# Kernel tuning notes

Measured on AMD Instinct MI355X. Metric: run time of the kernel, lower is better.

The kernel has to match this reference:

```python
import jax, jax.numpy as jnp
import numpy as np

B, S = 64, 1024
D_INPUT, D_POLAR, N_LAYERS, KAN, N_CLASSES = 256, 256, 8, 32, 1000
PI = float(np.pi)
EPS = 1e-8


def _gelu(v):
    return jax.nn.gelu(v, approximate=False)  # torch nn.GELU default = exact erf


def setup_inputs() -> dict:
    key = jax.random.key(0)
    ks = jax.random.split(key, 16)

    def rn(k, shape, fan_in):
        return jax.random.normal(k, shape, jnp.float32) / np.sqrt(fan_in)

    return {
        "x": jax.random.normal(ks[0], (B, S, D_INPUT), jnp.float32),
        "embed_w": rn(ks[1], (D_INPUT, 2 * D_POLAR), D_INPUT),
        "embed_b": jnp.zeros((2 * D_POLAR,), jnp.float32),
        "mag_w1": rn(ks[2], (N_LAYERS, 1, KAN), 1),
        "mag_b1": jnp.zeros((N_LAYERS, KAN), jnp.float32),
        "mag_w2": rn(ks[3], (N_LAYERS, KAN, 1), KAN),
        "mag_b2": jnp.zeros((N_LAYERS, 1), jnp.float32),
        "ph_w1": rn(ks[4], (N_LAYERS, 2, KAN), 2),
        "ph_b1": jnp.zeros((N_LAYERS, KAN), jnp.float32),
        "ph_w2": rn(ks[5], (N_LAYERS, KAN, 2), KAN),
        "ph_b2": jnp.zeros((N_LAYERS, 2), jnp.float32),
        "cls_w1": rn(ks[6], (D_POLAR, KAN), D_POLAR),
        "cls_b1": jnp.zeros((KAN,), jnp.float32),
        "cls_w2": rn(ks[7], (KAN, N_CLASSES), KAN),
        "cls_b2": jnp.zeros((N_CLASSES,), jnp.float32),
    }


def _forward(x, embed_w, embed_b, mag_w1, mag_b1, mag_w2, mag_b2,
             ph_w1, ph_b1, ph_w2, ph_b2, cls_w1, cls_b1, cls_w2, cls_b2):
    h = x @ embed_w + embed_b                      # [B,S,2D]
    r = jnp.abs(h[..., :D_POLAR]) + 0.1            # [B,S,D]
    theta = h[..., D_POLAR:] * PI                  # [B,S,D]
    for i in range(N_LAYERS):
        xc = r * jnp.cos(theta)
        yc = r * jnp.sin(theta)
        xm = xc.mean(axis=1, keepdims=True)        # [B,1,D]
        ym = yc.mean(axis=1, keepdims=True)
        r_agg = jnp.sqrt(xm * xm + ym * ym + EPS)
        th_agg = jnp.arctan2(ym, xm)
        # magnitude MLP (1 -> 32 -> 1) in log space, per channel
        log_r = jnp.log(r_agg + EPS)[..., None]    # [B,1,D,1]
        lr = _gelu(log_r @ mag_w1[i] + mag_b1[i]) @ mag_w2[i] + mag_b2[i]
        r_trans = jnp.exp(lr[..., 0])              # [B,1,D]
        # phase MLP (2 -> 32 -> 2) on (sin, cos)
        pin = jnp.stack([jnp.sin(th_agg), jnp.cos(th_agg)], axis=-1)  # [B,1,D,2]
        pout = _gelu(pin @ ph_w1[i] + ph_b1[i]) @ ph_w2[i] + ph_b2[i]
        norm = jnp.sqrt(pout[..., 0] ** 2 + pout[..., 1] ** 2 + EPS)
        th_trans = jnp.arctan2(pout[..., 0] / norm, pout[..., 1] / norm)
        x_out = xc + r_trans * jnp.cos(th_trans)
        y_out = yc + r_trans * jnp.sin(th_trans)
        r = jnp.sqrt(x_out * x_out + y_out * y_out + EPS)
        theta = jnp.arctan2(y_out, x_out)
    pooled = r.mean(axis=1)                        # [B,D]
    return _gelu(pooled @ cls_w1 + cls_b1) @ cls_w2 + cls_b2  # [B,n_classes]


def reference(x, embed_w, embed_b, mag_w1, mag_b1, mag_w2, mag_b2,
              ph_w1, ph_b1, ph_w2, ph_b2, cls_w1, cls_b1, cls_w2, cls_b2):
    return _forward(x, embed_w, embed_b, mag_w1, mag_b1, mag_w2, mag_b2,
                    ph_w1, ph_b1, ph_w2, ph_b2, cls_w1, cls_b1, cls_w2, cls_b2)
```

## Files before the change

### kernel.cpp

```cpp
#include <hip/hip_runtime.h>
#include <hip/hip_bf16.h>
#include <hip/hip_fp16.h>

#define EPS 1e-8f
#define PI_F 3.14159265358979323846f

typedef _Float16 half8 __attribute__((ext_vector_type(8)));
typedef _Float16 half4 __attribute__((ext_vector_type(4)));
typedef float f32x4 __attribute__((ext_vector_type(4)));
typedef float f32x2 __attribute__((ext_vector_type(2)));

__device__ __forceinline__ float gelu_exact(float v) {
    return 0.5f * v * (1.0f + erff(v * 0.70710678118654752f));
}

__global__ void convertW(const float* __restrict__ W,
                         _Float16* __restrict__ Wth, _Float16* __restrict__ Wtl,
                         float* __restrict__ zero_base) {
    int idx = blockIdx.x * 256 + threadIdx.x;
    if (idx < 49152) zero_base[idx] = 0.f;
    int col = idx & 511, k = idx >> 9;
    int d   = col & 255;
    int g   = d >> 6;
    int dl  = d & 63;
    int h12 = col >> 8;
    int r   = (dl >> 5) * 64 + ((dl & 1) + 2 * h12) * 16 + ((dl & 31) >> 1);
    int kt  = k >> 5, ko = k & 31;
    float f = W[k * 512 + col];
    _Float16 h = (_Float16)f;
    int o = ((g * 8 + kt) * 128 + r) * 32 + ko;
    Wth[o] = h;
    Wtl[o] = (_Float16)(f - (float)h);
}

__global__ __launch_bounds__(256) void gemm_embed(
    const float* __restrict__ x,
    const _Float16* __restrict__ Wth, const _Float16* __restrict__ Wtl,
    const float* __restrict__ bias,
    unsigned short* __restrict__ XY8,
    float* __restrict__ XMsum, float* __restrict__ YMsum)
{
    const int tid  = threadIdx.x;
    const int wave = tid >> 6;
    const int lane = tid & 63;
    const int wm   = wave >> 1;
    const int wn   = wave & 1;
    const int id   = blockIdx.x;
    const int xcd  = id & 7;
    const int s    = id >> 3;
    const int g    = s & 3;
    const int mt   = (s >> 2) * 8 + xcd;
    const int m0   = mt * 128;
    const int q    = lane >> 4, ln = lane & 15;

    f32x4 acc[4][4];
#pragma unroll
    for (int mi = 0; mi < 4; ++mi)
#pragma unroll
        for (int nt = 0; nt < 4; ++nt)
            acc[mi][nt] = (f32x4){0.f, 0.f, 0.f, 0.f};

    const float* xbase[4];
#pragma unroll
    for (int mi = 0; mi < 4; ++mi)
        xbase[mi] = x + (size_t)(m0 + wm * 64 + mi * 16 + ln) * 256 + q * 8;

    const _Float16* wb = Wth + (size_t)g * 32768 + (wn * 64 + ln) * 32 + q * 8;
    const _Float16* wl = Wtl + (size_t)g * 32768 + (wn * 64 + ln) * 32 + q * 8;

#pragma unroll 1
    for (int kt = 0; kt < 8; ++kt) {
        half8 bh[4], bl[4];
#pragma unroll
        for (int nt = 0; nt < 4; ++nt) {
            bh[nt] = *(const half8*)(wb + kt * 4096 + nt * 512);
            bl[nt] = *(const half8*)(wl + kt * 4096 + nt * 512);
        }
#pragma unroll
        for (int mi = 0; mi < 4; ++mi) {
            const float* src = xbase[mi] + kt * 32;
            const float4 f0 = *(const float4*)(src);
            const float4 f1 = *(const float4*)(src + 4);
            half8 hh, ll;
            hh[0] = (_Float16)f0.x; ll[0] = (_Float16)(f0.x - (float)hh[0]);
            hh[1] = (_Float16)f0.y; ll[1] = (_Float16)(f0.y - (float)hh[1]);
            hh[2] = (_Float16)f0.z; ll[2] = (_Float16)(f0.z - (float)hh[2]);
            hh[3] = (_Float16)f0.w; ll[3] = (_Float16)(f0.w - (float)hh[3]);
            hh[4] = (_Float16)f1.x; ll[4] = (_Float16)(f1.x - (float)hh[4]);
            hh[5] = (_Float16)f1.y; ll[5] = (_Float16)(f1.y - (float)hh[5]);
            hh[6] = (_Float16)f1.z; ll[6] = (_Float16)(f1.z - (float)hh[6]);
            hh[7] = (_Float16)f1.w; ll[7] = (_Float16)(f1.w - (float)hh[7]);
#pragma unroll
            for (int nt = 0; nt < 4; ++nt)
                acc[mi][nt] = __builtin_amdgcn_mfma_f32_16x16x32_f16(hh, bh[nt], acc[mi][nt], 0, 0, 0);
#pragma unroll
            for (int nt = 0; nt < 4; ++nt)
                acc[mi][nt] = __builtin_amdgcn_mfma_f32_16x16x32_f16(hh, bl[nt], acc[mi][nt], 0, 0, 0);
#pragma unroll
            for (int nt = 0; nt < 4; ++nt)
                acc[mi][nt] = __builtin_amdgcn_mfma_f32_16x16x32_f16(ll, bh[nt], acc[mi][nt], 0, 0, 0);
        }
    }

    const int d0 = g * 64 + wn * 32 + 2 * ln;
    const int b  = m0 >> 10;
    const float b1_0 = bias[d0],       b1_1 = bias[d0 + 1];
    const float b2_0 = bias[256 + d0], b2_1 = bias[256 + d0 + 1];
    float sx0 = 0.f, sy0 = 0.f, sx1 = 0.f, sy1 = 0.f;
#pragma unroll
    for (int mi = 0; mi < 4; ++mi) {
#pragma unroll
        for (int i = 0; i < 4; ++i) {
            const int row = m0 + wm * 64 + mi * 16 + q * 4 + i;
            const float h1a = acc[mi][0][i] + b1_0;
            const float h2a = acc[mi][2][i] + b2_0;
            const float rra = fabsf(h1a) + 0.1f;
            float sva, cva;
            __sincosf(PI_F * h2a, &sva, &cva);
            const float xca = rra * cva, yca = rra * sva;
            const float h1b = acc[mi][1][i] + b1_1;
            const float h2b = acc[mi][3][i] + b2_1;
            const float rrb = fabsf(h1b) + 0.1f;
            float svb, cvb;
            __sincosf(PI_F * h2b, &svb, &cvb);
            const float xcb = rrb * cvb, ycb = rrb * svb;
            int pk = __builtin_amdgcn_cvt_pk_fp8_f32(xca, yca, 0, false);
            pk = __builtin_amdgcn_cvt_pk_fp8_f32(xcb, ycb, pk, true);
            *(unsigned int*)(XY8 + (size_t)row * 256 + d0) = (unsigned int)pk;
            sx0 += xca; sy0 += yca;
            sx1 += xcb; sy1 += ycb;
        }
    }
    sx0 += __shfl_down(sx0, 32); sx0 += __shfl_down(sx0, 16);
    sy0 += __shfl_down(sy0, 32); sy0 += __shfl_down(sy0, 16);
    sx1 += __shfl_down(sx1, 32); sx1 += __shfl_down(sx1, 16);
    sy1 += __shfl_down(sy1, 32); sy1 += __shfl_down(sy1, 16);
    if (lane < 16) {
        atomicAdd(&XMsum[b * 256 + d0], sx0);
        atomicAdd(&YMsum[b * 256 + d0], sy0);
        atomicAdd(&XMsum[b * 256 + d0 + 1], sx1);
        atomicAdd(&YMsum[b * 256 + d0 + 1], sy1);
    }
}

__global__ __launch_bounds__(256) void layers_kernel(
    const float* __restrict__ XMsum, const float* __restrict__ YMsum,
    const float* __restrict__ mw1, const float* __restrict__ mb1,
    const float* __restrict__ mw2, const float* __restrict__ mb2,
    const float* __restrict__ pw1, const float* __restrict__ pb1,
    const float* __restrict__ pw2, const float* __restrict__ pb2,
    float* __restrict__ DX, float* __restrict__ DY)
{
    __shared__ float s_mw1[256], s_mb1[256], s_mw2[256], s_mb2[8];
    __shared__ float s_pw1[512], s_pb1[256], s_pw2[512], s_pb2[16];
    const int tid = threadIdx.x;
    s_mw1[tid] = mw1[tid]; s_mb1[tid] = mb1[tid];
    s_mw2[tid] = mw2[tid]; s_pb1[tid] = pb1[tid];
    s_pw1[tid] = pw1[tid]; s_pw1[256 + tid] = pw1[256 + tid];
    s_pw2[tid] = pw2[tid]; s_pw2[256 + tid] = pw2[256 + tid];
    if (tid < 8)  s_mb2[tid] = mb2[tid];
    if (tid < 16) s_pb2[tid] = pb2[tid];
    __syncthreads();

    const int gid = blockIdx.x * 256 + tid;
    const int idx = gid >> 3;
    const int sub = gid & 7;
    float xm = XMsum[idx] * (1.0f / 1024.0f);
    float ym = YMsum[idx] * (1.0f / 1024.0f);
    float dxa = 0.f, dya = 0.f;
#pragma unroll 1
    for (int i = 0; i < 8; ++i) {
        float r2    = xm * xm + ym * ym;
        float r_agg = sqrtf(r2 + EPS);
        float hyp   = sqrtf(r2);
        float inv   = hyp > 0.f ? 1.0f / hyp : 0.f;
        float st    = ym * inv;
        float ct    = hyp > 0.f ? xm * inv : 1.0f;
        float log_r = logf(r_agg + EPS);
        float lr = 0.f, p0 = 0.f, p1 = 0.f;
#pragma unroll
        for (int k4 = 0; k4 < 4; ++k4) {
            int k = sub * 4 + k4;
            float hm = gelu_exact(log_r * s_mw1[i * 32 + k] + s_mb1[i * 32 + k]);
            lr += hm * s_mw2[i * 32 + k];
            float hp = gelu_exact(st * s_pw1[i * 64 + k] + ct * s_pw1[i * 64 + 32 + k] + s_pb1[i * 32 + k]);
            p0 += hp * s_pw2[i * 64 + 2 * k + 0];
            p1 += hp * s_pw2[i * 64 + 2 * k + 1];
        }
        lr += __shfl_xor(lr, 1); lr += __shfl_xor(lr, 2); lr += __shfl_xor(lr, 4);
        p0 += __shfl_xor(p0, 1); p0 += __shfl_xor(p0, 2); p0 += __shfl_xor(p0, 4);
        p1 += __shfl_xor(p1, 1); p1 += __shfl_xor(p1, 2); p1 += __shfl_xor(p1, 4);
        lr += s_mb2[i];
        p0 += s_pb2[i * 2 + 0];
        p1 += s_pb2[i * 2 + 1];
        float r_trans = expf(lr);
        float hp2  = sqrtf(p0 * p0 + p1 * p1);
        float invp = hp2 > 0.f ? 1.0f / hp2 : 0.f;
        float ctt  = hp2 > 0.f ? p1 * invp : 1.0f;
        float stt  = p0 * invp;
        float dx = r_trans * ctt;
        float dy = r_trans * stt;
        dxa += dx; dya += dy; xm += dx; ym += dy;
    }
    if (sub == 0) { DX[idx] = dxa; DY[idx] = dya; }
}

__global__ __launch_bounds__(256) void pool_kernel(
    const unsigned short* __restrict__ XY8,
    const float* __restrict__ DX, const float* __restrict__ DY,
    float* __restrict__ pooled)
{
    __shared__ float red[256][9];
    const int b = blockIdx.x, sc = blockIdx.y, tid = threadIdx.x;
    const int dg = tid & 31;
    const int sh = tid >> 5;
    const int d0 = dg * 8;
    float dxv[8], dyv[8], s[8];
#pragma unroll
    for (int j = 0; j < 8; ++j) {
        dxv[j] = DX[b * 256 + d0 + j];
        dyv[j] = DY[b * 256 + d0 + j];
        s[j] = 0.f;
    }
    const int r0 = sc * 128 + sh * 16;
    const size_t base = ((size_t)b * 1024 + r0) * 256 + d0;
#pragma unroll 4
    for (int i = 0; i < 16; ++i) {
        const int4 v = *(const int4*)(XY8 + base + (size_t)i * 256);
        const int wv[4] = {v.x, v.y, v.z, v.w};
#pragma unroll
        for (int w = 0; w < 4; ++w) {
            f32x2 pa = __builtin_amdgcn_cvt_pk_f32_fp8(wv[w], false);
            f32x2 pb = __builtin_amdgcn_cvt_pk_f32_fp8(wv[w], true);
            float xa = pa[0] + dxv[2 * w],     ya = pa[1] + dyv[2 * w];
            float xb = pb[0] + dxv[2 * w + 1], yb = pb[1] + dyv[2 * w + 1];
            s[2 * w]     += sqrtf(xa * xa + ya * ya + EPS);
            s[2 * w + 1] += sqrtf(xb * xb + yb * yb + EPS);
        }
    }
#pragma unroll
    for (int j = 0; j < 8; ++j) red[tid][j] = s[j];
    __syncthreads();
    if (tid < 32) {
#pragma unroll
        for (int j = 0; j < 8; ++j) {
            float t = 0.f;
#pragma unroll
            for (int c = 0; c < 8; ++c) t += red[c * 32 + tid][j];
            atomicAdd(&pooled[b * 256 + tid * 8 + j], t);
        }
    }
}

__global__ __launch_bounds__(256) void cls_kernel(
    const float* __restrict__ pooled,
    const float* __restrict__ w1, const float* __restrict__ b1,
    const float* __restrict__ w2, const float* __restrict__ b2,
    float* __restrict__ out)
{
    __shared__ float pl[256];
    __shared__ float part[8][32];
    __shared__ float hd[32];
    const int b = blockIdx.x, yc = blockIdx.y, tid = threadIdx.x;
    pl[tid] = pooled[b * 256 + tid] * (1.0f / 1024.0f);
    __syncthreads();
    const int hu = tid & 31, kc = tid >> 5;
    float a = 0.f;
    for (int k = kc * 32; k < kc * 32 + 32; ++k) a += pl[k] * w1[k * 32 + hu];
    part[kc][hu] = a;
    __syncthreads();
    if (tid < 32) {
        float s = b1[tid];
#pragma unroll
        for (int c = 0; c < 8; ++c) s += part[c][tid];
        hd[tid] = gelu_exact(s);
    }
    __syncthreads();
    const int n0 = yc * 250;
    const int nend = (n0 + 250 < 1000) ? n0 + 250 : 1000;
    for (int n = n0 + tid; n < nend; n += 256) {
        float s = b2[n];
#pragma unroll
        for (int k = 0; k < 32; ++k) s += hd[k] * w2[k * 1000 + n];
        out[b * 1000 + n] = s;
    }
}

extern "C" void kernel_launch(void* const* d_in, const int* in_sizes, int n_in,
                              void* d_out, int out_size, void* d_ws, size_t ws_size,
                              hipStream_t stream)
{
    const float* x       = (const float*)d_in[0];
    const float* embed_w = (const float*)d_in[1];
    const float* embed_b = (const float*)d_in[2];
    const float* mag_w1  = (const float*)d_in[3];
    const float* mag_b1  = (const float*)d_in[4];
    const float* mag_w2  = (const float*)d_in[5];
    const float* mag_b2  = (const float*)d_in[6];
    const float* ph_w1   = (const float*)d_in[7];
    const float* ph_b1   = (const float*)d_in[8];
    const float* ph_w2   = (const float*)d_in[9];
    const float* ph_b2   = (const float*)d_in[10];
    const float* cls_w1  = (const float*)d_in[11];
    const float* cls_b1  = (const float*)d_in[12];
    const float* cls_w2  = (const float*)d_in[13];
    const float* cls_b2  = (const float*)d_in[14];
    float* out = (float*)d_out;

    char* ws = (char*)d_ws;
    unsigned short* XY8 = (unsigned short*)(ws + 0);
    _Float16* Wth = (_Float16*)(ws + 33554432);
    _Float16* Wtl = (_Float16*)(ws + 33816576);
    float* XMsum  = (float*)(ws + 34078720);
    float* YMsum  = (float*)(ws + 34144256);
    float* pooled = (float*)(ws + 34209792);
    float* DX     = (float*)(ws + 34275328);
    float* DY     = (float*)(ws + 34340864);

    convertW<<<512, 256, 0, stream>>>(embed_w, Wth, Wtl, XMsum);
    gemm_embed<<<2048, 256, 0, stream>>>(x, Wth, Wtl, embed_b, XY8, XMsum, YMsum);
    layers_kernel<<<512, 256, 0, stream>>>(XMsum, YMsum, mag_w1, mag_b1, mag_w2, mag_b2,
                                           ph_w1, ph_b1, ph_w2, ph_b2, DX, DY);
    pool_kernel<<<dim3(64, 8), 256, 0, stream>>>(XY8, DX, DY, pooled);
    cls_kernel<<<dim3(64, 4), 256, 0, stream>>>(pooled, cls_w1, cls_b1, cls_w2, cls_b2, out);
}
```

Measured before the change: 239.5 us.

## Stage embed GEMM input tiles through double-buffered swizzled LDS with async loads

The embedding GEMM previously had each wave read its fp32 x rows straight from global memory, so the two column-waves sharing a row block fetched the same data twice. Now the whole 128x32 fp32 tile is copied once per block into LDS with global_load_lds, using an XOR swizzle to avoid bank conflicts. Two LDS buffers let the next k-step's copy run while the current one is being converted and fed to MFMA. The launch bounds also now request 4 blocks per CU. The cost is 32 KB of LDS per block and a barrier each k-step, both of which may limit occupancy.

```diff
diff --git a/kernel.cpp b/kernel.cpp
--- a/kernel.cpp
+++ b/kernel.cpp
@@ -12,6 +12,12 @@
 
 __device__ __forceinline__ float gelu_exact(float v) {
     return 0.5f * v * (1.0f + erff(v * 0.70710678118654752f));
+}
+
+__device__ __forceinline__ void load_lds16(const float* g, float* l) {
+    __builtin_amdgcn_global_load_lds(
+        (const __attribute__((address_space(1))) void*)g,
+        (__attribute__((address_space(3))) void*)l, 16, 0, 0);
 }
 
 __global__ void convertW(const float* __restrict__ W,
@@ -33,13 +39,14 @@
     Wtl[o] = (_Float16)(f - (float)h);
 }
 
-__global__ __launch_bounds__(256) void gemm_embed(
+__global__ __launch_bounds__(256, 4) void gemm_embed(
     const float* __restrict__ x,
     const _Float16* __restrict__ Wth, const _Float16* __restrict__ Wtl,
     const float* __restrict__ bias,
     unsigned short* __restrict__ XY8,
     float* __restrict__ XMsum, float* __restrict__ YMsum)
 {
+    __shared__ __attribute__((aligned(16))) float A32[2][4096];
     const int tid  = threadIdx.x;
     const int wave = tid >> 6;
     const int lane = tid & 63;
@@ -60,27 +67,44 @@
         for (int nt = 0; nt < 4; ++nt)
             acc[mi][nt] = (f32x4){0.f, 0.f, 0.f, 0.f};
 
-    const float* xbase[4];
-#pragma unroll
-    for (int mi = 0; mi < 4; ++mi)
-        xbase[mi] = x + (size_t)(m0 + wm * 64 + mi * 16 + ln) * 256 + q * 8;
+    const float* srcp[4];
+#pragma unroll
+    for (int n = 0; n < 4; ++n) {
+        const int G  = wave * 256 + n * 64 + lane;
+        const int r  = G >> 3;
+        const int gp = G & 7;
+        srcp[n] = x + (size_t)(m0 + r) * 256 + ((gp ^ (r & 7)) * 4);
+    }
+
+#define STAGE(KT, C)                                                          \
+    {                                                                         \
+        float* lb_ = &A32[C][wave * 1024];                                    \
+        _Pragma("unroll")                                                     \
+        for (int n = 0; n < 4; ++n)                                           \
+            load_lds16(srcp[n] + (KT) * 32, lb_ + n * 256);                   \
+    }
 
     const _Float16* wb = Wth + (size_t)g * 32768 + (wn * 64 + ln) * 32 + q * 8;
     const _Float16* wl = Wtl + (size_t)g * 32768 + (wn * 64 + ln) * 32 + q * 8;
 
+    STAGE(0, 0);
+
 #pragma unroll 1
     for (int kt = 0; kt < 8; ++kt) {
+        const int c = kt & 1;
         half8 bh[4], bl[4];
 #pragma unroll
         for (int nt = 0; nt < 4; ++nt) {
             bh[nt] = *(const half8*)(wb + kt * 4096 + nt * 512);
             bl[nt] = *(const half8*)(wl + kt * 4096 + nt * 512);
         }
+        __syncthreads();
+        if (kt < 7) STAGE(kt + 1, c ^ 1);
 #pragma unroll
         for (int mi = 0; mi < 4; ++mi) {
-            const float* src = xbase[mi] + kt * 32;
-            const float4 f0 = *(const float4*)(src);
-            const float4 f1 = *(const float4*)(src + 4);
+            const int r = wm * 64 + mi * 16 + ln;
+            const float4 f0 = *(const float4*)&A32[c][r * 32 + ((2 * q)     ^ (r & 7)) * 4];
+            const float4 f1 = *(const float4*)&A32[c][r * 32 + ((2 * q + 1) ^ (r & 7)) * 4];
             half8 hh, ll;
             hh[0] = (_Float16)f0.x; ll[0] = (_Float16)(f0.x - (float)hh[0]);
             hh[1] = (_Float16)f0.y; ll[1] = (_Float16)(f0.y - (float)hh[1]);
@@ -101,6 +125,7 @@
                 acc[mi][nt] = __builtin_amdgcn_mfma_f32_16x16x32_f16(ll, bh[nt], acc[mi][nt], 0, 0, 0);
         }
     }
+#undef STAGE
 
     const int d0 = g * 64 + wn * 32 + 2 * ln;
     const int b  = m0 >> 10;
```

New measurement: 210.7 us. 12.0% less time.

## Fuse all stages into one cooperative persistent kernel and stage A tiles through LDS

Applied to the files above, without the earlier changes.

Replaces the five separate launches with a single cooperative kernel of 1024 blocks that runs weight conversion, GEMM, layers, pooling and the classifier, separated by grid-wide syncs, with the old multi-launch path kept as a fallback if the cooperative launch fails. The GEMM now has each block cooperatively load and split the x tile into fp16 hi/lo parts in swizzled shared memory, then read MFMA fragments from there instead of every wave converting its own rows. The aim is to cut launch gaps and redundant global loads and conversions. In exchange it adds grid-sync overhead, leaves most blocks idle in the later phases, and caps occupancy with launch bounds of 4 blocks per CU.

```diff
diff --git a/kernel.cpp b/kernel.cpp
--- a/kernel.cpp
+++ b/kernel.cpp
@@ -1,12 +1,14 @@
 #include <hip/hip_runtime.h>
+#include <hip/hip_cooperative_groups.h>
 #include <hip/hip_bf16.h>
 #include <hip/hip_fp16.h>
 
 #define EPS 1e-8f
 #define PI_F 3.14159265358979323846f
 
+namespace cg = cooperative_groups;
+
 typedef _Float16 half8 __attribute__((ext_vector_type(8)));
-typedef _Float16 half4 __attribute__((ext_vector_type(4)));
 typedef float f32x4 __attribute__((ext_vector_type(4)));
 typedef float f32x2 __attribute__((ext_vector_type(2)));
 
@@ -14,10 +16,12 @@
     return 0.5f * v * (1.0f + erff(v * 0.70710678118654752f));
 }
 
-__global__ void convertW(const float* __restrict__ W,
-                         _Float16* __restrict__ Wth, _Float16* __restrict__ Wtl,
-                         float* __restrict__ zero_base) {
-    int idx = blockIdx.x * 256 + threadIdx.x;
+
+__device__ __forceinline__ void convert_body(
+    int idx, const float* __restrict__ W,
+    _Float16* __restrict__ Wth, _Float16* __restrict__ Wtl,
+    float* __restrict__ zero_base)
+{
     if (idx < 49152) zero_base[idx] = 0.f;
     int col = idx & 511, k = idx >> 9;
     int d   = col & 255;
@@ -33,19 +37,18 @@
     Wtl[o] = (_Float16)(f - (float)h);
 }
 
-__global__ __launch_bounds__(256) void gemm_embed(
+__device__ __forceinline__ void gemm_unit(
+    int id, int tid, _Float16* Ah, _Float16* Al,
     const float* __restrict__ x,
     const _Float16* __restrict__ Wth, const _Float16* __restrict__ Wtl,
     const float* __restrict__ bias,
     unsigned short* __restrict__ XY8,
     float* __restrict__ XMsum, float* __restrict__ YMsum)
 {
-    const int tid  = threadIdx.x;
     const int wave = tid >> 6;
     const int lane = tid & 63;
     const int wm   = wave >> 1;
     const int wn   = wave & 1;
-    const int id   = blockIdx.x;
     const int xcd  = id & 7;
     const int s    = id >> 3;
     const int g    = s & 3;
@@ -60,11 +63,6 @@
         for (int nt = 0; nt < 4; ++nt)
             acc[mi][nt] = (f32x4){0.f, 0.f, 0.f, 0.f};
 
-    const float* xbase[4];
-#pragma unroll
-    for (int mi = 0; mi < 4; ++mi)
-        xbase[mi] = x + (size_t)(m0 + wm * 64 + mi * 16 + ln) * 256 + q * 8;
-
     const _Float16* wb = Wth + (size_t)g * 32768 + (wn * 64 + ln) * 32 + q * 8;
     const _Float16* wl = Wtl + (size_t)g * 32768 + (wn * 64 + ln) * 32 + q * 8;
 
@@ -76,9 +74,12 @@
             bh[nt] = *(const half8*)(wb + kt * 4096 + nt * 512);
             bl[nt] = *(const half8*)(wl + kt * 4096 + nt * 512);
         }
-#pragma unroll
-        for (int mi = 0; mi < 4; ++mi) {
-            const float* src = xbase[mi] + kt * 32;
+        __syncthreads();
+#pragma unroll
+        for (int L = 0; L < 2; ++L) {
+            int idx2 = L * 256 + tid;
+            int r = idx2 >> 2, cq = idx2 & 3;
+            const float* src = x + (size_t)(m0 + r) * 256 + kt * 32 + cq * 8;
             const float4 f0 = *(const float4*)(src);
             const float4 f1 = *(const float4*)(src + 4);
             half8 hh, ll;
@@ -90,15 +91,35 @@
             hh[5] = (_Float16)f1.y; ll[5] = (_Float16)(f1.y - (float)hh[5]);
             hh[6] = (_Float16)f1.z; ll[6] = (_Float16)(f1.z - (float)hh[6]);
             hh[7] = (_Float16)f1.w; ll[7] = (_Float16)(f1.w - (float)hh[7]);
+            int pos = cq ^ ((r >> 1) & 3);
+            *(half8*)&Ah[r * 32 + pos * 8] = hh;
+            *(half8*)&Al[r * 32 + pos * 8] = ll;
+        }
+        __syncthreads();
+
+        half8 am[4];
+#pragma unroll
+        for (int mi = 0; mi < 4; ++mi) {
+            int row = wm * 64 + mi * 16 + ln;
+            am[mi] = *(const half8*)&Ah[row * 32 + (q ^ ((row >> 1) & 3)) * 8];
+        }
+#pragma unroll
+        for (int mi = 0; mi < 4; ++mi)
 #pragma unroll
             for (int nt = 0; nt < 4; ++nt)
-                acc[mi][nt] = __builtin_amdgcn_mfma_f32_16x16x32_f16(hh, bh[nt], acc[mi][nt], 0, 0, 0);
+                acc[mi][nt] = __builtin_amdgcn_mfma_f32_16x16x32_f16(am[mi], bh[nt], acc[mi][nt], 0, 0, 0);
+#pragma unroll
+        for (int mi = 0; mi < 4; ++mi)
 #pragma unroll
             for (int nt = 0; nt < 4; ++nt)
-                acc[mi][nt] = __builtin_amdgcn_mfma_f32_16x16x32_f16(hh, bl[nt], acc[mi][nt], 0, 0, 0);
+                acc[mi][nt] = __builtin_amdgcn_mfma_f32_16x16x32_f16(am[mi], bl[nt], acc[mi][nt], 0, 0, 0);
+#pragma unroll
+        for (int mi = 0; mi < 4; ++mi) {
+            int row = wm * 64 + mi * 16 + ln;
+            half8 alv = *(const half8*)&Al[row * 32 + (q ^ ((row >> 1) & 3)) * 8];
 #pragma unroll
             for (int nt = 0; nt < 4; ++nt)
-                acc[mi][nt] = __builtin_amdgcn_mfma_f32_16x16x32_f16(ll, bh[nt], acc[mi][nt], 0, 0, 0);
+                acc[mi][nt] = __builtin_amdgcn_mfma_f32_16x16x32_f16(alv, bh[nt], acc[mi][nt], 0, 0, 0);
         }
     }
 
@@ -143,7 +164,8 @@
     }
 }
 
-__global__ __launch_bounds__(256) void layers_kernel(
+__device__ __forceinline__ void layers_body(
+    int bid, int tid, float* sm,
     const float* __restrict__ XMsum, const float* __restrict__ YMsum,
     const float* __restrict__ mw1, const float* __restrict__ mb1,
     const float* __restrict__ mw2, const float* __restrict__ mb2,
@@ -151,18 +173,15 @@
     const float* __restrict__ pw2, const float* __restrict__ pb2,
     float* __restrict__ DX, float* __restrict__ DY)
 {
-    __shared__ float s_mw1[256], s_mb1[256], s_mw2[256], s_mb2[8];
-    __shared__ float s_pw1[512], s_pb1[256], s_pw2[512], s_pb2[16];
-    const int tid = threadIdx.x;
-    s_mw1[tid] = mw1[tid]; s_mb1[tid] = mb1[tid];
-    s_mw2[tid] = mw2[tid]; s_pb1[tid] = pb1[tid];
-    s_pw1[tid] = pw1[tid]; s_pw1[256 + tid] = pw1[256 + tid];
-    s_pw2[tid] = pw2[tid]; s_pw2[256 + tid] = pw2[256 + tid];
-    if (tid < 8)  s_mb2[tid] = mb2[tid];
-    if (tid < 16) s_pb2[tid] = pb2[tid];
+    sm[tid] = mw1[tid]; sm[256 + tid] = mb1[tid];
+    sm[512 + tid] = mw2[tid]; sm[768 + tid] = pb1[tid];
+    sm[1024 + tid] = pw1[tid]; sm[1280 + tid] = pw1[256 + tid];
+    sm[1536 + tid] = pw2[tid]; sm[1792 + tid] = pw2[256 + tid];
+    if (tid < 8)  sm[2048 + tid] = mb2[tid];
+    if (tid < 16) sm[2056 + tid] = pb2[tid];
     __syncthreads();
 
-    const int gid = blockIdx.x * 256 + tid;
+    const int gid = bid * 256 + tid;
     const int idx = gid >> 3;
     const int sub = gid & 7;
     float xm = XMsum[idx] * (1.0f / 1024.0f);
@@ -181,18 +200,18 @@
 #pragma unroll
         for (int k4 = 0; k4 < 4; ++k4) {
             int k = sub * 4 + k4;
-            float hm = gelu_exact(log_r * s_mw1[i * 32 + k] + s_mb1[i * 32 + k]);
-            lr += hm * s_mw2[i * 32 + k];
-            float hp = gelu_exact(st * s_pw1[i * 64 + k] + ct * s_pw1[i * 64 + 32 + k] + s_pb1[i * 32 + k]);
-            p0 += hp * s_pw2[i * 64 + 2 * k + 0];
-            p1 += hp * s_pw2[i * 64 + 2 * k + 1];
+            float hm = gelu_exact(log_r * sm[i * 32 + k] + sm[256 + i * 32 + k]);
+            lr += hm * sm[512 + i * 32 + k];
+            float hp = gelu_exact(st * sm[1024 + i * 64 + k] + ct * sm[1024 + i * 64 + 32 + k] + sm[768 + i * 32 + k]);
+            p0 += hp * sm[1536 + i * 64 + 2 * k + 0];
+            p1 += hp * sm[1536 + i * 64 + 2 * k + 1];
         }
         lr += __shfl_xor(lr, 1); lr += __shfl_xor(lr, 2); lr += __shfl_xor(lr, 4);
         p0 += __shfl_xor(p0, 1); p0 += __shfl_xor(p0, 2); p0 += __shfl_xor(p0, 4);
         p1 += __shfl_xor(p1, 1); p1 += __shfl_xor(p1, 2); p1 += __shfl_xor(p1, 4);
-        lr += s_mb2[i];
-        p0 += s_pb2[i * 2 + 0];
-        p1 += s_pb2[i * 2 + 1];
+        lr += sm[2048 + i];
+        p0 += sm[2056 + i * 2 + 0];
+        p1 += sm[2056 + i * 2 + 1];
         float r_trans = expf(lr);
         float hp2  = sqrtf(p0 * p0 + p1 * p1);
         float invp = hp2 > 0.f ? 1.0f / hp2 : 0.f;
@@ -205,13 +224,12 @@
     if (sub == 0) { DX[idx] = dxa; DY[idx] = dya; }
 }
 
-__global__ __launch_bounds__(256) void pool_kernel(
+__device__ __forceinline__ void pool_body(
+    int b, int sc, int tid, float (*red)[9],
     const unsigned short* __restrict__ XY8,
     const float* __restrict__ DX, const float* __restrict__ DY,
     float* __restrict__ pooled)
 {
-    __shared__ float red[256][9];
-    const int b = blockIdx.x, sc = blockIdx.y, tid = threadIdx.x;
     const int dg = tid & 31;
     const int sh = tid >> 5;
     const int d0 = dg * 8;
@@ -252,28 +270,25 @@
     }
 }
 
-__global__ __launch_bounds__(256) void cls_kernel(
+__device__ __forceinline__ void cls_body(
+    int b, int yc, int tid, float* smf,
     const float* __restrict__ pooled,
     const float* __restrict__ w1, const float* __restrict__ b1,
     const float* __restrict__ w2, const float* __restrict__ b2,
     float* __restrict__ out)
 {
-    __shared__ float pl[256];
-    __shared__ float part[8][32];
-    __shared__ float hd[32];
-    const int b = blockIdx.x, yc = blockIdx.y, tid = threadIdx.x;
-    pl[tid] = pooled[b * 256 + tid] * (1.0f / 1024.0f);
+    smf[tid] = pooled[b * 256 + tid] * (1.0f / 1024.0f);
     __syncthreads();
     const int hu = tid & 31, kc = tid >> 5;
     float a = 0.f;
-    for (int k = kc * 32; k < kc * 32 + 32; ++k) a += pl[k] * w1[k * 32 + hu];
-    part[kc][hu] = a;
+    for (int k = kc * 32; k < kc * 32 + 32; ++k) a += smf[k] * w1[k * 32 + hu];
+    smf[256 + kc * 32 + hu] = a;
     __syncthreads();
     if (tid < 32) {
         float s = b1[tid];
 #pragma unroll
-        for (int c = 0; c < 8; ++c) s += part[c][tid];
-        hd[tid] = gelu_exact(s);
+        for (int c = 0; c < 8; ++c) s += smf[256 + c * 32 + tid];
+        smf[512 + tid] = gelu_exact(s);
     }
     __syncthreads();
     const int n0 = yc * 250;
@@ -281,9 +296,105 @@
     for (int n = n0 + tid; n < nend; n += 256) {
         float s = b2[n];
 #pragma unroll
-        for (int k = 0; k < 32; ++k) s += hd[k] * w2[k * 1000 + n];
+        for (int k = 0; k < 32; ++k) s += smf[512 + k] * w2[k * 1000 + n];
         out[b * 1000 + n] = s;
     }
+}
+
+__global__ __launch_bounds__(256, 4) void fused_all(
+    const float* __restrict__ x, const float* __restrict__ embed_w,
+    const float* __restrict__ embed_b,
+    const float* __restrict__ mw1, const float* __restrict__ mb1,
+    const float* __restrict__ mw2, const float* __restrict__ mb2,
+    const float* __restrict__ pw1, const float* __restrict__ pb1,
+    const float* __restrict__ pw2, const float* __restrict__ pb2,
+    const float* __restrict__ cw1, const float* __restrict__ cb1,
+    const float* __restrict__ cw2, const float* __restrict__ cb2,
+    float* __restrict__ out,
+    unsigned short* __restrict__ XY8,
+    _Float16* __restrict__ Wth, _Float16* __restrict__ Wtl,
+    float* __restrict__ XMsum, float* __restrict__ YMsum,
+    float* __restrict__ pooled, float* __restrict__ DX, float* __restrict__ DY)
+{
+    cg::grid_group grid = cg::this_grid();
+    __shared__ __attribute__((aligned(16))) char smem[16384];
+    const int bid = blockIdx.x, tid = threadIdx.x;
+
+    {
+        int idx = bid * 256 + tid;
+        if (idx < 131072) convert_body(idx, embed_w, Wth, Wtl, XMsum);
+    }
+    grid.sync();
+
+    {
+        _Float16* Ah = (_Float16*)smem;
+        _Float16* Al = Ah + 4096;
+#pragma unroll 1
+        for (int u = 0; u < 2; ++u)
+            gemm_unit(bid + u * 1024, tid, Ah, Al, x, Wth, Wtl, embed_b, XY8, XMsum, YMsum);
+    }
+    grid.sync();
+
+    if (bid < 512)
+        layers_body(bid, tid, (float*)smem, XMsum, YMsum,
+                    mw1, mb1, mw2, mb2, pw1, pb1, pw2, pb2, DX, DY);
+    grid.sync();
+
+    if (bid < 512)
+        pool_body(bid >> 3, bid & 7, tid, (float(*)[9])smem, XY8, DX, DY, pooled);
+    grid.sync();
+
+    if (bid < 256)
+        cls_body(bid >> 2, bid & 3, tid, (float*)smem, pooled, cw1, cb1, cw2, cb2, out);
+}
+
+__global__ __launch_bounds__(256) void convertW_k(
+    const float* __restrict__ W, _Float16* __restrict__ Wth,
+    _Float16* __restrict__ Wtl, float* __restrict__ zero_base)
+{
+    convert_body(blockIdx.x * 256 + threadIdx.x, W, Wth, Wtl, zero_base);
+}
+
+__global__ __launch_bounds__(256, 4) void gemm_k(
+    const float* __restrict__ x, const _Float16* __restrict__ Wth,
+    const _Float16* __restrict__ Wtl, const float* __restrict__ bias,
+    unsigned short* __restrict__ XY8, float* __restrict__ XMsum,
+    float* __restrict__ YMsum)
+{
+    __shared__ __attribute__((aligned(16))) _Float16 Ah[4096], Al[4096];
+    gemm_unit(blockIdx.x, threadIdx.x, Ah, Al, x, Wth, Wtl, bias, XY8, XMsum, YMsum);
+}
+
+__global__ __launch_bounds__(256) void layers_k(
+    const float* __restrict__ XMsum, const float* __restrict__ YMsum,
+    const float* __restrict__ mw1, const float* __restrict__ mb1,
+    const float* __restrict__ mw2, const float* __restrict__ mb2,
+    const float* __restrict__ pw1, const float* __restrict__ pb1,
+    const float* __restrict__ pw2, const float* __restrict__ pb2,
+    float* __restrict__ DX, float* __restrict__ DY)
+{
+    __shared__ float sm[2072];
+    layers_body(blockIdx.x, threadIdx.x, sm, XMsum, YMsum,
+                mw1, mb1, mw2, mb2, pw1, pb1, pw2, pb2, DX, DY);
+}
+
+__global__ __launch_bounds__(256) void pool_k(
+    const unsigned short* __restrict__ XY8,
+    const float* __restrict__ DX, const float* __restrict__ DY,
+    float* __restrict__ pooled)
+{
+    __shared__ float red[256][9];
+    pool_body(blockIdx.x, blockIdx.y, threadIdx.x, red, XY8, DX, DY, pooled);
+}
+
+__global__ __launch_bounds__(256) void cls_k(
+    const float* __restrict__ pooled,
+    const float* __restrict__ w1, const float* __restrict__ b1,
+    const float* __restrict__ w2, const float* __restrict__ b2,
+    float* __restrict__ out)
+{
+    __shared__ float smf[544];
+    cls_body(blockIdx.x, blockIdx.y, threadIdx.x, smf, pooled, w1, b1, w2, b2, out);
 }
 
 extern "C" void kernel_launch(void* const* d_in, const int* in_sizes, int n_in,
@@ -317,10 +428,26 @@
     float* DX     = (float*)(ws + 34275328);
     float* DY     = (float*)(ws + 34340864);
 
-    convertW<<<512, 256, 0, stream>>>(embed_w, Wth, Wtl, XMsum);
-    gemm_embed<<<2048, 256, 0, stream>>>(x, Wth, Wtl, embed_b, XY8, XMsum, YMsum);
-    layers_kernel<<<512, 256, 0, stream>>>(XMsum, YMsum, mag_w1, mag_b1, mag_w2, mag_b2,
-                                           ph_w1, ph_b1, ph_w2, ph_b2, DX, DY);
-    pool_kernel<<<dim3(64, 8), 256, 0, stream>>>(XY8, DX, DY, pooled);
-    cls_kernel<<<dim3(64, 4), 256, 0, stream>>>(pooled, cls_w1, cls_b1, cls_w2, cls_b2, out);
-}
+    void* args[] = {
+        (void*)&x, (void*)&embed_w, (void*)&embed_b,
+        (void*)&mag_w1, (void*)&mag_b1, (void*)&mag_w2, (void*)&mag_b2,
+        (void*)&ph_w1, (void*)&ph_b1, (void*)&ph_w2, (void*)&ph_b2,
+        (void*)&cls_w1, (void*)&cls_b1, (void*)&cls_w2, (void*)&cls_b2,
+        (void*)&out,
+        (void*)&XY8, (void*)&Wth, (void*)&Wtl,
+        (void*)&XMsum, (void*)&YMsum, (void*)&pooled, (void*)&DX, (void*)&DY
+    };
+
+    hipError_t err = hipLaunchCooperativeKernel(
+        (void*)fused_all, dim3(1024), dim3(256), args, 0, stream);
+
+    if (err != hipSuccess) {
+        (void)hipGetLastError();
+        convertW_k<<<512, 256, 0, stream>>>(embed_w, Wth, Wtl, XMsum);
+        gemm_k<<<2048, 256, 0, stream>>>(x, Wth, Wtl, embed_b, XY8, XMsum, YMsum);
+        layers_k<<<512, 256, 0, stream>>>(XMsum, YMsum, mag_w1, mag_b1, mag_w2, mag_b2,
+                                          ph_w1, ph_b1, ph_w2, ph_b2, DX, DY);
+        pool_k<<<dim3(64, 8), 256, 0, stream>>>(XY8, DX, DY, pooled);
+        cls_k<<<dim3(64, 4), 256, 0, stream>>>(pooled, cls_w1, cls_b1, cls_w2, cls_b2, out);
+    }
+}
```

Result: slower. 646.7 us (+170.0%).
